# Kernel optimization log

Hardware: AMD Instinct MI355X
Metric: run time of the kernel (lower is better)

## Reference

```python
import jax, jax.numpy as jnp
import numpy as np

# Module hyperparameters (from init_kwargs / submodule semantics)
B, N, C, H = 32, 1024, 192, 3
D = C // H                      # head_dim = 64
TAU_MIN = 0.1                   # LearnableTemperature: tau = tau_min + softplus(p)
P_MAX = 0.3                     # LearnedHeadDropout: rate = p_max * sigmoid(logit)
ANNEAL_START = 2.0              # TemperatureScheduler: mult = start -> 1 over training
TRAIN_PROGRESS = 0.5            # scalar forward arg (fixed)


def setup_inputs() -> dict:
    key = jax.random.key(0)
    ks = jax.random.split(key, 8)
    x = jax.random.normal(ks[0], (B, N, C), jnp.float32)
    qkv_w = jax.random.normal(ks[1], (3 * C, C), jnp.float32) * 0.02
    qkv_b = jnp.zeros((3 * C,), jnp.float32)
    proj_w = jax.random.normal(ks[2], (C, C), jnp.float32) * 0.02
    proj_b = jnp.zeros((C,), jnp.float32)
    temp_param = jax.random.normal(ks[3], (H,), jnp.float32) * 0.1
    dropout_logits = jax.random.normal(ks[4], (H,), jnp.float32) * 0.1
    residual_param = jnp.zeros((), jnp.float32)
    tau_aleatoric = jax.random.uniform(ks[5], (B, H), jnp.float32) * 0.5
    return {"x": x, "qkv_w": qkv_w, "qkv_b": qkv_b, "proj_w": proj_w,
            "proj_b": proj_b, "temp_param": temp_param,
            "dropout_logits": dropout_logits, "residual_param": residual_param,
            "tau_aleatoric": tau_aleatoric}


def reference(x, qkv_w, qkv_b, proj_w, proj_b, temp_param, dropout_logits,
              residual_param, tau_aleatoric):
    b, n, c = x.shape
    scale = D ** -0.5
    # QKV projection -> (3, B, H, N, D)
    qkv = (x @ qkv_w.T + qkv_b).reshape(b, n, 3, H, D).transpose(2, 0, 3, 1, 4)
    q, k, v = qkv[0], qkv[1], qkv[2]
    # epistemic per-head temperature with curriculum annealing
    tau_e = TAU_MIN + jax.nn.softplus(temp_param)            # (H,)
    anneal = ANNEAL_START - (ANNEAL_START - 1.0) * TRAIN_PROGRESS
    tau_e = tau_e * anneal
    # combine with aleatoric temperature: (B, H, 1, 1)
    tau = tau_aleatoric[:, :, None, None] + tau_e[None, :, None, None]
    # attention scores with per-head temperature scaling
    attn = jnp.einsum('bhnd,bhmd->bhnm', q, k) * scale / tau  # (B,H,N,N)
    attn = jax.nn.softmax(attn, axis=-1)
    # early-exit confidence: mean over heads and queries of max attn prob
    confidence = attn.max(axis=-1).mean(axis=(1, 2))          # (B,)
    # learned head dropout (deterministic eval form: scale by keep prob)
    keep = 1.0 - P_MAX * jax.nn.sigmoid(dropout_logits)       # (H,)
    attn_d = attn * keep[None, :, None, None]
    # attention output + projection
    out = jnp.einsum('bhnm,bhmd->bnhd', attn_d, v).reshape(b, n, c)
    out = out @ proj_w.T + proj_b
    # learned residual blend
    w = jax.nn.sigmoid(residual_param)
    out = w * out + (1.0 - w) * x
    return out, confidence
```

## Files before the change

### kernel.cpp

```cpp
#include <hip/hip_runtime.h>

#define BB 32
#define NN 1024
#define CC 192
#define HH 3
#define DD 64
#define BHND 6291456

typedef __bf16 bf16x8 __attribute__((ext_vector_type(8)));
typedef float  f32x4  __attribute__((ext_vector_type(4)));

__device__ __align__(16) unsigned short g_q  [BHND];
__device__ __align__(16) unsigned short g_k  [BHND];
__device__ __align__(16) unsigned short g_vt [BHND];
__device__ __align__(16) unsigned short g_ao [BHND];
__device__ __align__(16) unsigned short g_wb [3 * CC * CC];
__device__ __align__(16) unsigned short g_pwb[CC * CC];
__device__ float g_conf[BB];

__device__ __forceinline__ unsigned short f2b(float f) {
    union { float f; unsigned int i; } z; z.f = f;
    return (unsigned short)((z.i + 0x7fffu + ((z.i >> 16) & 1u)) >> 16);
}

__global__ __launch_bounds__(256) void convert_kernel(
    const float* __restrict__ qw, const float* __restrict__ pw)
{
    const int i = blockIdx.x * 256 + threadIdx.x;
    if (blockIdx.x == 0 && threadIdx.x < BB) g_conf[threadIdx.x] = 0.0f;
    float4 v; unsigned short* dst;
    if (i < 27648) { v = ((const float4*)qw)[i];         dst = g_wb  + i * 4; }
    else           { v = ((const float4*)pw)[i - 27648]; dst = g_pwb + (i - 27648) * 4; }
    const unsigned int a = (unsigned int)f2b(v.x) | ((unsigned int)f2b(v.y) << 16);
    const unsigned int b = (unsigned int)f2b(v.z) | ((unsigned int)f2b(v.w) << 16);
    *(uint2*)dst = make_uint2(a, b);
}

__global__ __launch_bounds__(256) void qkv_kernel(
    const float* __restrict__ x,
    const float* __restrict__ bias,
    const float* __restrict__ tp,
    const float* __restrict__ ta)
{
    const int tid  = threadIdx.x;
    const int wv   = tid >> 6;
    const int lane = tid & 63;
    const int q    = lane >> 4;
    const int mq   = lane & 15;
    const int base = blockIdx.x * 128;
    const int r0a  = base + wv * 16;
    const int r0b  = r0a + 64;
    const int b    = base >> 10;

    float mult_h[HH];
    #pragma unroll
    for (int h = 0; h < HH; ++h) {
        const float tau_e = (0.1f + logf(1.0f + __expf(tp[h]))) * 1.5f;
        mult_h[h] = 0.125f / (ta[b * 3 + h] + tau_e);
    }

    bf16x8 af0[6], af1[6];
    #pragma unroll
    for (int kh = 0; kh < 6; ++kh) {
        #pragma unroll
        for (int s = 0; s < 2; ++s) {
            const int row = (s ? r0b : r0a) + mq;
            const float4 u0 = *(const float4*)(x + (size_t)row * CC + kh * 32 + q * 8);
            const float4 u1 = *(const float4*)(x + (size_t)row * CC + kh * 32 + q * 8 + 4);
            union { bf16x8 v; unsigned short s_[8]; } t;
            t.s_[0] = f2b(u0.x); t.s_[1] = f2b(u0.y); t.s_[2] = f2b(u0.z); t.s_[3] = f2b(u0.w);
            t.s_[4] = f2b(u1.x); t.s_[5] = f2b(u1.y); t.s_[6] = f2b(u1.z); t.s_[7] = f2b(u1.w);
            if (s) af1[kh] = t.v; else af0[kh] = t.v;
        }
    }

    bf16x8 bcur[6];
    #pragma unroll
    for (int kh = 0; kh < 6; ++kh)
        bcur[kh] = *(const bf16x8*)(g_wb + (size_t)mq * CC + kh * 32 + q * 8);
    #pragma unroll 2
    for (int ot = 0; ot < 24; ++ot) {
        const int o0 = ot * 16;
        bf16x8 bnxt[6];
        if (ot < 23) {
            #pragma unroll
            for (int kh = 0; kh < 6; ++kh)
                bnxt[kh] = *(const bf16x8*)(g_wb + (size_t)(o0 + 16 + mq) * CC + kh * 32 + q * 8);
        }
        f32x4 acc0 = (f32x4){0.f,0.f,0.f,0.f}, acc1 = (f32x4){0.f,0.f,0.f,0.f};
        #pragma unroll
        for (int kh = 0; kh < 6; ++kh) {
            acc0 = __builtin_amdgcn_mfma_f32_16x16x32_bf16(af0[kh], bcur[kh], acc0, 0, 0, 0);
            acc1 = __builtin_amdgcn_mfma_f32_16x16x32_bf16(af1[kh], bcur[kh], acc1, 0, 0, 0);
        }
        const float bv = bias[o0 + mq];
        if (ot < 12) {
            const int h = o0 >> 6, d0 = o0 & 63;
            const float m = mult_h[h];
            unsigned short* d0p = g_q + ((size_t)((b * 3 + h) * NN + (r0a & 1023) + q * 4)) * DD + d0 + mq;
            unsigned short* d1p = g_q + ((size_t)((b * 3 + h) * NN + (r0b & 1023) + q * 4)) * DD + d0 + mq;
            #pragma unroll
            for (int r = 0; r < 4; ++r) {
                d0p[(size_t)r * DD] = f2b((acc0[r] + bv) * m);
                d1p[(size_t)r * DD] = f2b((acc1[r] + bv) * m);
            }
        } else {
            const int oo = o0 - 192;
            const int h = oo >> 6, d0 = oo & 63;
            unsigned short* d0p = g_k + ((size_t)((b * 3 + h) * NN + (r0a & 1023) + q * 4)) * DD + d0 + mq;
            unsigned short* d1p = g_k + ((size_t)((b * 3 + h) * NN + (r0b & 1023) + q * 4)) * DD + d0 + mq;
            #pragma unroll
            for (int r = 0; r < 4; ++r) {
                d0p[(size_t)r * DD] = f2b(acc0[r] + bv);
                d1p[(size_t)r * DD] = f2b(acc1[r] + bv);
            }
        }
        #pragma unroll
        for (int kh = 0; kh < 6; ++kh) bcur[kh] = bnxt[kh];
    }

    #pragma unroll
    for (int kh = 0; kh < 6; ++kh)
        bcur[kh] = *(const bf16x8*)(g_wb + (size_t)(384 + mq) * CC + kh * 32 + q * 8);
    #pragma unroll 2
    for (int ot = 0; ot < 12; ++ot) {
        const int dd0 = ot * 16;
        bf16x8 bnxt[6];
        if (ot < 11) {
            #pragma unroll
            for (int kh = 0; kh < 6; ++kh)
                bnxt[kh] = *(const bf16x8*)(g_wb + (size_t)(384 + dd0 + 16 + mq) * CC + kh * 32 + q * 8);
        }
        f32x4 acc0 = (f32x4){0.f,0.f,0.f,0.f}, acc1 = (f32x4){0.f,0.f,0.f,0.f};
        #pragma unroll
        for (int kh = 0; kh < 6; ++kh) {
            acc0 = __builtin_amdgcn_mfma_f32_16x16x32_bf16(bcur[kh], af0[kh], acc0, 0, 0, 0);
            acc1 = __builtin_amdgcn_mfma_f32_16x16x32_bf16(bcur[kh], af1[kh], acc1, 0, 0, 0);
        }
        #pragma unroll
        for (int r = 0; r < 4; ++r) {
            const int dd = dd0 + q * 4 + r;
            const int h = dd >> 6, d = dd & 63;
            const float bv = bias[384 + dd];
            g_vt[((size_t)((b * 3 + h) * DD + d)) * NN + (r0a & 1023) + mq] = f2b(acc0[r] + bv);
            g_vt[((size_t)((b * 3 + h) * DD + d)) * NN + (r0b & 1023) + mq] = f2b(acc1[r] + bv);
        }
        #pragma unroll
        for (int kh = 0; kh < 6; ++kh) bcur[kh] = bnxt[kh];
    }
}

__global__ __launch_bounds__(256, 3) void attn_kernel(
    const float* __restrict__ dl)
{
    const int tid  = threadIdx.x;
    const int wv   = tid >> 6;
    const int lane = tid & 63;
    const int q    = lane >> 4;
    const int mq   = lane & 15;

    const int bh = blockIdx.x >> 3;
    const int n0 = (blockIdx.x & 7) * 128;
    const int b  = bh / 3;
    const int h  = bh - b * 3;
    const float keep = 1.0f - 0.3f / (1.0f + __expf(-dl[h]));

    __shared__ __align__(16) unsigned short ks[2][4096];
    __shared__ __align__(16) unsigned short vt[2][4096];
    __shared__ __align__(16) unsigned short pt[8192];
    __shared__ float conf_s[128];

    const size_t qra = (size_t)(bh * NN + n0 + wv * 16 + mq) * DD;
    const size_t qrb = qra + (size_t)64 * DD;
    const bf16x8 qfa0 = *(const bf16x8*)(g_q + qra + q * 8);
    const bf16x8 qfa1 = *(const bf16x8*)(g_q + qra + 32 + q * 8);
    const bf16x8 qfb0 = *(const bf16x8*)(g_q + qrb + q * 8);
    const bf16x8 qfb1 = *(const bf16x8*)(g_q + qrb + 32 + q * 8);

    const size_t krow0 = (size_t)(bh * NN + wv * 16 + mq) * DD;
    const size_t vrow  = (size_t)(bh * DD + wv * 16 + mq) * NN;
    bf16x8 kr0 = *(const bf16x8*)(g_k + krow0 + q * 8);
    bf16x8 kr1 = *(const bf16x8*)(g_k + krow0 + 32 + q * 8);
    bf16x8 vr0 = *(const bf16x8*)(g_vt + vrow + q * 8);
    bf16x8 vr1 = *(const bf16x8*)(g_vt + vrow + 32 + q * 8);

    f32x4 oa[4], ob[4];
    #pragma unroll
    for (int i = 0; i < 4; ++i) { oa[i] = (f32x4){0.f,0.f,0.f,0.f}; ob[i] = (f32x4){0.f,0.f,0.f,0.f}; }
    float la = 0.0f, lb = 0.0f, pma = 0.0f, pmb = 0.0f;

    for (int it = 0; it < 16; ++it) {
        const int cur = it & 1;
        ((bf16x8*)ks[cur])[tid]       = kr0;
        ((bf16x8*)ks[cur])[256 + tid] = kr1;
        ((bf16x8*)vt[cur])[tid]       = vr0;
        ((bf16x8*)vt[cur])[256 + tid] = vr1;
        if (it < 15) {
            const int t1 = (it + 1) * 64;
            kr0 = *(const bf16x8*)(g_k + krow0 + (size_t)t1 * DD + q * 8);
            kr1 = *(const bf16x8*)(g_k + krow0 + (size_t)t1 * DD + 32 + q * 8);
            vr0 = *(const bf16x8*)(g_vt + vrow + t1 + q * 8);
            vr1 = *(const bf16x8*)(g_vt + vrow + t1 + 32 + q * 8);
        }
        __syncthreads();

        f32x4 sa[4], sb[4];
        #pragma unroll
        for (int i = 0; i < 4; ++i) { sa[i] = (f32x4){0.f,0.f,0.f,0.f}; sb[i] = (f32x4){0.f,0.f,0.f,0.f}; }
        #pragma unroll
        for (int kh = 0; kh < 2; ++kh) {
            const bf16x8 qfa = kh ? qfa1 : qfa0;
            const bf16x8 qfb = kh ? qfb1 : qfb0;
            #pragma unroll
            for (int kt = 0; kt < 4; ++kt) {
                const bf16x8 afr = ((const bf16x8*)ks[cur])[kh * 256 + kt * 64 + lane];
                sa[kt] = __builtin_amdgcn_mfma_f32_16x16x32_bf16(afr, qfa, sa[kt], 0, 0, 0);
                sb[kt] = __builtin_amdgcn_mfma_f32_16x16x32_bf16(afr, qfb, sb[kt], 0, 0, 0);
            }
        }

        #pragma unroll
        for (int s = 0; s < 2; ++s) {
            unsigned short* ptb = pt + s * 4096;
            #pragma unroll
            for (int kt = 0; kt < 4; ++kt) {
                const f32x4 sv = s ? sb[kt] : sa[kt];
                const float p0 = __expf(sv[0]);
                const float p1 = __expf(sv[1]);
                const float p2 = __expf(sv[2]);
                const float p3 = __expf(sv[3]);
                const float mx = fmaxf(fmaxf(p0, p1), fmaxf(p2, p3));
                if (s) { pmb = fmaxf(pmb, mx); lb += (p0 + p1) + (p2 + p3); }
                else   { pma = fmaxf(pma, mx); la += (p0 + p1) + (p2 + p3); }
                const unsigned int ua = (__float_as_uint(p0) >> 16) | (__float_as_uint(p1) & 0xffff0000u);
                const unsigned int ub = (__float_as_uint(p2) >> 16) | (__float_as_uint(p3) & 0xffff0000u);
                const int kh2   = kt >> 1;
                const int qk    = (kt * 2 + (q >> 1)) & 3;
                const int chunk = ((wv * 2 + kh2) * 4 + qk) * 16 + mq;
                *(uint2*)((char*)ptb + chunk * 16 + (q & 1) * 8) = make_uint2(ua, ub);
            }
        }
        __builtin_amdgcn_s_waitcnt(0xC07F);

        #pragma unroll
        for (int kh = 0; kh < 2; ++kh) {
            const bf16x8 pfa = ((const bf16x8*)pt)[(wv * 2 + kh) * 64 + lane];
            const bf16x8 pfb = ((const bf16x8*)(pt + 4096))[(wv * 2 + kh) * 64 + lane];
            #pragma unroll
            for (int ctv = 0; ctv < 4; ++ctv) {
                const bf16x8 vf = ((const bf16x8*)vt[cur])[kh * 256 + ctv * 64 + lane];
                oa[ctv] = __builtin_amdgcn_mfma_f32_16x16x32_bf16(pfa, vf, oa[ctv], 0, 0, 0);
                ob[ctv] = __builtin_amdgcn_mfma_f32_16x16x32_bf16(pfb, vf, ob[ctv], 0, 0, 0);
            }
        }
    }

    float l0 = la, l1 = lb;
    l0 += __shfl_xor(l0, 16, 64); l0 += __shfl_xor(l0, 32, 64);
    l1 += __shfl_xor(l1, 16, 64); l1 += __shfl_xor(l1, 32, 64);
    float p0 = pma, p1 = pmb;
    p0 = fmaxf(p0, __shfl_xor(p0, 16, 64)); p0 = fmaxf(p0, __shfl_xor(p0, 32, 64));
    p1 = fmaxf(p1, __shfl_xor(p1, 16, 64)); p1 = fmaxf(p1, __shfl_xor(p1, 32, 64));
    const float invla = 1.0f / l0;
    const float invlb = 1.0f / l1;

    if (lane < 16) {
        conf_s[wv * 16 + mq]      = p0 * invla;
        conf_s[64 + wv * 16 + mq] = p1 * invlb;
    }
    __syncthreads();
    if (tid < 64) {
        float v = conf_s[tid] + conf_s[64 + tid];
        #pragma unroll
        for (int off = 1; off <= 32; off <<= 1) v += __shfl_xor(v, off, 64);
        if (tid == 0) atomicAdd(&g_conf[b], v);
    }

    #pragma unroll
    for (int s = 0; s < 2; ++s) {
        const float invl = s ? invlb : invla;
        float sc[4];
        #pragma unroll
        for (int r = 0; r < 4; ++r)
            sc[r] = keep * __int_as_float(
                __builtin_amdgcn_ds_bpermute((q * 4 + r) << 2, __float_as_int(invl)));
        #pragma unroll
        for (int ctv = 0; ctv < 4; ++ctv)
            #pragma unroll
            for (int r = 0; r < 4; ++r) {
                const f32x4 o = s ? ob[ctv] : oa[ctv];
                g_ao[((size_t)(b * NN + n0 + s * 64 + wv * 16 + q * 4 + r)) * CC + h * DD + ctv * 16 + mq] =
                    f2b(o[r] * sc[r]);
            }
    }
}

__global__ __launch_bounds__(256) void proj_kernel(
    const float* __restrict__ pb,
    const float* __restrict__ rp,
    const float* __restrict__ x,
    float* __restrict__ out,
    float* __restrict__ out_c)
{
    const int tid  = threadIdx.x;
    const int wv   = tid >> 6;
    const int lane = tid & 63;
    const int q    = lane >> 4;
    const int mq   = lane & 15;
    const int base = blockIdx.x * 128;
    const int r0a  = base + wv * 16;
    const int r0b  = r0a + 64;

    if (blockIdx.x == 0 && tid < BB)
        out_c[tid] = g_conf[tid] * (1.0f / (float)(HH * NN));

    const float wres = 1.0f / (1.0f + __expf(-rp[0]));

    bf16x8 af0[6], af1[6];
    #pragma unroll
    for (int kh = 0; kh < 6; ++kh) {
        af0[kh] = *(const bf16x8*)(g_ao + (size_t)(r0a + mq) * CC + kh * 32 + q * 8);
        af1[kh] = *(const bf16x8*)(g_ao + (size_t)(r0b + mq) * CC + kh * 32 + q * 8);
    }

    bf16x8 bcur[6];
    #pragma unroll
    for (int kh = 0; kh < 6; ++kh)
        bcur[kh] = *(const bf16x8*)(g_pwb + (size_t)mq * CC + kh * 32 + q * 8);
    #pragma unroll 2
    for (int ot = 0; ot < 12; ++ot) {
        const int o0 = ot * 16;
        bf16x8 bnxt[6];
        if (ot < 11) {
            #pragma unroll
            for (int kh = 0; kh < 6; ++kh)
                bnxt[kh] = *(const bf16x8*)(g_pwb + (size_t)(o0 + 16 + mq) * CC + kh * 32 + q * 8);
        }
        f32x4 acc0 = (f32x4){0.f,0.f,0.f,0.f}, acc1 = (f32x4){0.f,0.f,0.f,0.f};
        #pragma unroll
        for (int kh = 0; kh < 6; ++kh) {
            acc0 = __builtin_amdgcn_mfma_f32_16x16x32_bf16(af0[kh], bcur[kh], acc0, 0, 0, 0);
            acc1 = __builtin_amdgcn_mfma_f32_16x16x32_bf16(af1[kh], bcur[kh], acc1, 0, 0, 0);
        }
        const float bv = pb[o0 + mq];
        #pragma unroll
        for (int r = 0; r < 4; ++r) {
            const int na = r0a + q * 4 + r;
            const int nb = r0b + q * 4 + r;
            const float xa = x[(size_t)na * CC + o0 + mq];
            const float xb = x[(size_t)nb * CC + o0 + mq];
            out[(size_t)na * CC + o0 + mq] = wres * (acc0[r] + bv) + (1.0f - wres) * xa;
            out[(size_t)nb * CC + o0 + mq] = wres * (acc1[r] + bv) + (1.0f - wres) * xb;
        }
        #pragma unroll
        for (int kh = 0; kh < 6; ++kh) bcur[kh] = bnxt[kh];
    }
}

extern "C" void kernel_launch(void* const* d_in, const int* in_sizes, int n_in,
                              void* d_out, int out_size, void* d_ws, size_t ws_size,
                              hipStream_t stream)
{
    const float* x  = (const float*)d_in[0];
    const float* qw = (const float*)d_in[1];
    const float* qb = (const float*)d_in[2];
    const float* pw = (const float*)d_in[3];
    const float* pb = (const float*)d_in[4];
    const float* tp = (const float*)d_in[5];
    const float* dl = (const float*)d_in[6];
    const float* rp = (const float*)d_in[7];
    const float* ta = (const float*)d_in[8];

    float* out   = (float*)d_out;
    float* out_c = out + (size_t)BB * NN * CC;

    convert_kernel<<<144, 256, 0, stream>>>(qw, pw);
    qkv_kernel<<<(BB * NN) / 128, 256, 0, stream>>>(x, qb, tp, ta);
    attn_kernel<<<BB * HH * (NN / 128), 256, 0, stream>>>(dl);
    proj_kernel<<<(BB * NN) / 128, 256, 0, stream>>>(pb, rp, x, out, out_c);
}
```

Baseline: 182.4 us.

## Split QKV and projection GEMMs across more blocks and remap attention grid

Result: no change. 185.8 us (+1.9%).

```diff
diff --git a/kernel.cpp b/kernel.cpp
--- a/kernel.cpp
+++ b/kernel.cpp
@@ -47,17 +47,12 @@
     const int lane = tid & 63;
     const int q    = lane >> 4;
     const int mq   = lane & 15;
-    const int base = blockIdx.x * 128;
+    const int rg   = blockIdx.x / 3;
+    const int cg   = blockIdx.x - rg * 3;
+    const int base = rg * 128;
     const int r0a  = base + wv * 16;
     const int r0b  = r0a + 64;
     const int b    = base >> 10;
-
-    float mult_h[HH];
-    #pragma unroll
-    for (int h = 0; h < HH; ++h) {
-        const float tau_e = (0.1f + logf(1.0f + __expf(tp[h]))) * 1.5f;
-        mult_h[h] = 0.125f / (ta[b * 3 + h] + tau_e);
-    }
 
     bf16x8 af0[6], af1[6];
     #pragma unroll
@@ -74,79 +69,78 @@
         }
     }
 
+    const int wrow0 = cg * 192;
+
     bf16x8 bcur[6];
     #pragma unroll
     for (int kh = 0; kh < 6; ++kh)
-        bcur[kh] = *(const bf16x8*)(g_wb + (size_t)mq * CC + kh * 32 + q * 8);
-    #pragma unroll 2
-    for (int ot = 0; ot < 24; ++ot) {
-        const int o0 = ot * 16;
-        bf16x8 bnxt[6];
-        if (ot < 23) {
-            #pragma unroll
-            for (int kh = 0; kh < 6; ++kh)
-                bnxt[kh] = *(const bf16x8*)(g_wb + (size_t)(o0 + 16 + mq) * CC + kh * 32 + q * 8);
-        }
-        f32x4 acc0 = (f32x4){0.f,0.f,0.f,0.f}, acc1 = (f32x4){0.f,0.f,0.f,0.f};
-        #pragma unroll
-        for (int kh = 0; kh < 6; ++kh) {
-            acc0 = __builtin_amdgcn_mfma_f32_16x16x32_bf16(af0[kh], bcur[kh], acc0, 0, 0, 0);
-            acc1 = __builtin_amdgcn_mfma_f32_16x16x32_bf16(af1[kh], bcur[kh], acc1, 0, 0, 0);
-        }
-        const float bv = bias[o0 + mq];
-        if (ot < 12) {
+        bcur[kh] = *(const bf16x8*)(g_wb + (size_t)(wrow0 + mq) * CC + kh * 32 + q * 8);
+
+    if (cg < 2) {
+        float mult_h[HH];
+        if (cg == 0) {
+            #pragma unroll
+            for (int h = 0; h < HH; ++h) {
+                const float tau_e = (0.1f + logf(1.0f + __expf(tp[h]))) * 1.5f;
+                mult_h[h] = 0.125f / (ta[b * 3 + h] + tau_e);
+            }
+        }
+        unsigned short* gout = cg == 0 ? g_q : g_k;
+        #pragma unroll 2
+        for (int ot = 0; ot < 12; ++ot) {
+            const int o0 = ot * 16;
+            bf16x8 bnxt[6];
+            if (ot < 11) {
+                #pragma unroll
+                for (int kh = 0; kh < 6; ++kh)
+                    bnxt[kh] = *(const bf16x8*)(g_wb + (size_t)(wrow0 + o0 + 16 + mq) * CC + kh * 32 + q * 8);
+            }
+            f32x4 acc0 = (f32x4){0.f,0.f,0.f,0.f}, acc1 = (f32x4){0.f,0.f,0.f,0.f};
+            #pragma unroll
+            for (int kh = 0; kh < 6; ++kh) {
+                acc0 = __builtin_amdgcn_mfma_f32_16x16x32_bf16(af0[kh], bcur[kh], acc0, 0, 0, 0);
+                acc1 = __builtin_amdgcn_mfma_f32_16x16x32_bf16(af1[kh], bcur[kh], acc1, 0, 0, 0);
+            }
+            const float bv = bias[wrow0 + o0 + mq];
             const int h = o0 >> 6, d0 = o0 & 63;
-            const float m = mult_h[h];
-            unsigned short* d0p = g_q + ((size_t)((b * 3 + h) * NN + (r0a & 1023) + q * 4)) * DD + d0 + mq;
-            unsigned short* d1p = g_q + ((size_t)((b * 3 + h) * NN + (r0b & 1023) + q * 4)) * DD + d0 + mq;
+            const float m = cg == 0 ? mult_h[h] : 1.0f;
+            unsigned short* d0p = gout + ((size_t)((b * 3 + h) * NN + (r0a & 1023) + q * 4)) * DD + d0 + mq;
+            unsigned short* d1p = gout + ((size_t)((b * 3 + h) * NN + (r0b & 1023) + q * 4)) * DD + d0 + mq;
             #pragma unroll
             for (int r = 0; r < 4; ++r) {
                 d0p[(size_t)r * DD] = f2b((acc0[r] + bv) * m);
                 d1p[(size_t)r * DD] = f2b((acc1[r] + bv) * m);
             }
-        } else {
-            const int oo = o0 - 192;
-            const int h = oo >> 6, d0 = oo & 63;
-            unsigned short* d0p = g_k + ((size_t)((b * 3 + h) * NN + (r0a & 1023) + q * 4)) * DD + d0 + mq;
-            unsigned short* d1p = g_k + ((size_t)((b * 3 + h) * NN + (r0b & 1023) + q * 4)) * DD + d0 + mq;
+            #pragma unroll
+            for (int kh = 0; kh < 6; ++kh) bcur[kh] = bnxt[kh];
+        }
+    } else {
+        #pragma unroll 2
+        for (int ot = 0; ot < 12; ++ot) {
+            const int dd0 = ot * 16;
+            bf16x8 bnxt[6];
+            if (ot < 11) {
+                #pragma unroll
+                for (int kh = 0; kh < 6; ++kh)
+                    bnxt[kh] = *(const bf16x8*)(g_wb + (size_t)(384 + dd0 + 16 + mq) * CC + kh * 32 + q * 8);
+            }
+            f32x4 acc0 = (f32x4){0.f,0.f,0.f,0.f}, acc1 = (f32x4){0.f,0.f,0.f,0.f};
+            #pragma unroll
+            for (int kh = 0; kh < 6; ++kh) {
+                acc0 = __builtin_amdgcn_mfma_f32_16x16x32_bf16(bcur[kh], af0[kh], acc0, 0, 0, 0);
+                acc1 = __builtin_amdgcn_mfma_f32_16x16x32_bf16(bcur[kh], af1[kh], acc1, 0, 0, 0);
+            }
             #pragma unroll
             for (int r = 0; r < 4; ++r) {
-                d0p[(size_t)r * DD] = f2b(acc0[r] + bv);
-                d1p[(size_t)r * DD] = f2b(acc1[r] + bv);
-            }
-        }
-        #pragma unroll
-        for (int kh = 0; kh < 6; ++kh) bcur[kh] = bnxt[kh];
-    }
-
-    #pragma unroll
-    for (int kh = 0; kh < 6; ++kh)
-        bcur[kh] = *(const bf16x8*)(g_wb + (size_t)(384 + mq) * CC + kh * 32 + q * 8);
-    #pragma unroll 2
-    for (int ot = 0; ot < 12; ++ot) {
-        const int dd0 = ot * 16;
-        bf16x8 bnxt[6];
-        if (ot < 11) {
-            #pragma unroll
-            for (int kh = 0; kh < 6; ++kh)
-                bnxt[kh] = *(const bf16x8*)(g_wb + (size_t)(384 + dd0 + 16 + mq) * CC + kh * 32 + q * 8);
-        }
-        f32x4 acc0 = (f32x4){0.f,0.f,0.f,0.f}, acc1 = (f32x4){0.f,0.f,0.f,0.f};
-        #pragma unroll
-        for (int kh = 0; kh < 6; ++kh) {
-            acc0 = __builtin_amdgcn_mfma_f32_16x16x32_bf16(bcur[kh], af0[kh], acc0, 0, 0, 0);
-            acc1 = __builtin_amdgcn_mfma_f32_16x16x32_bf16(bcur[kh], af1[kh], acc1, 0, 0, 0);
-        }
-        #pragma unroll
-        for (int r = 0; r < 4; ++r) {
-            const int dd = dd0 + q * 4 + r;
-            const int h = dd >> 6, d = dd & 63;
-            const float bv = bias[384 + dd];
-            g_vt[((size_t)((b * 3 + h) * DD + d)) * NN + (r0a & 1023) + mq] = f2b(acc0[r] + bv);
-            g_vt[((size_t)((b * 3 + h) * DD + d)) * NN + (r0b & 1023) + mq] = f2b(acc1[r] + bv);
-        }
-        #pragma unroll
-        for (int kh = 0; kh < 6; ++kh) bcur[kh] = bnxt[kh];
+                const int dd = dd0 + q * 4 + r;
+                const int h = dd >> 6, d = dd & 63;
+                const float bv = bias[384 + dd];
+                g_vt[((size_t)((b * 3 + h) * DD + d)) * NN + (r0a & 1023) + mq] = f2b(acc0[r] + bv);
+                g_vt[((size_t)((b * 3 + h) * DD + d)) * NN + (r0b & 1023) + mq] = f2b(acc1[r] + bv);
+            }
+            #pragma unroll
+            for (int kh = 0; kh < 6; ++kh) bcur[kh] = bnxt[kh];
+        }
     }
 }
 
@@ -159,10 +153,13 @@
     const int q    = lane >> 4;
     const int mq   = lane & 15;
 
-    const int bh = blockIdx.x >> 3;
-    const int n0 = (blockIdx.x & 7) * 128;
-    const int b  = bh / 3;
-    const int h  = bh - b * 3;
+    const int low3 = blockIdx.x & 7;
+    const int mid  = blockIdx.x >> 3;
+    const int tile = mid & 7;
+    const int bh   = (mid >> 3) * 8 + low3;
+    const int n0   = tile * 128;
+    const int b    = bh / 3;
+    const int h    = bh - b * 3;
     const float keep = 1.0f - 0.3f / (1.0f + __expf(-dl[h]));
 
     __shared__ __align__(16) unsigned short ks[2][4096];
@@ -307,9 +304,12 @@
     const int lane = tid & 63;
     const int q    = lane >> 4;
     const int mq   = lane & 15;
-    const int base = blockIdx.x * 128;
+    const int rg   = blockIdx.x >> 1;
+    const int cg   = blockIdx.x & 1;
+    const int base = rg * 128;
     const int r0a  = base + wv * 16;
     const int r0b  = r0a + 64;
+    const int ob0  = cg * 96;
 
     if (blockIdx.x == 0 && tid < BB)
         out_c[tid] = g_conf[tid] * (1.0f / (float)(HH * NN));
@@ -326,12 +326,12 @@
     bf16x8 bcur[6];
     #pragma unroll
     for (int kh = 0; kh < 6; ++kh)
-        bcur[kh] = *(const bf16x8*)(g_pwb + (size_t)mq * CC + kh * 32 + q * 8);
+        bcur[kh] = *(const bf16x8*)(g_pwb + (size_t)(ob0 + mq) * CC + kh * 32 + q * 8);
     #pragma unroll 2
-    for (int ot = 0; ot < 12; ++ot) {
-        const int o0 = ot * 16;
+    for (int ot = 0; ot < 6; ++ot) {
+        const int o0 = ob0 + ot * 16;
         bf16x8 bnxt[6];
-        if (ot < 11) {
+        if (ot < 5) {
             #pragma unroll
             for (int kh = 0; kh < 6; ++kh)
                 bnxt[kh] = *(const bf16x8*)(g_pwb + (size_t)(o0 + 16 + mq) * CC + kh * 32 + q * 8);
@@ -375,7 +375,7 @@
     float* out_c = out + (size_t)BB * NN * CC;
 
     convert_kernel<<<144, 256, 0, stream>>>(qw, pw);
-    qkv_kernel<<<(BB * NN) / 128, 256, 0, stream>>>(x, qb, tp, ta);
+    qkv_kernel<<<(BB * NN) / 128 * 3, 256, 0, stream>>>(x, qb, tp, ta);
     attn_kernel<<<BB * HH * (NN / 128), 256, 0, stream>>>(dl);
-    proj_kernel<<<(BB * NN) / 128, 256, 0, stream>>>(pb, rp, x, out, out_c);
-}
+    proj_kernel<<<(BB * NN) / 128 * 2, 256, 0, stream>>>(pb, rp, x, out, out_c);
+}
```
